# Kernel optimization log

Measured on AMD Instinct MI355X. Metric: run time of the kernel, lower is better.

The kernel has to match this reference:

```python
import jax, jax.numpy as jnp
import numpy as np

B, H, W, C, UNITS = 16, 64, 64, 64, 128

def setup_inputs() -> dict:
    key = jax.random.key(0)
    k1, k2 = jax.random.split(key)
    x = jax.random.normal(k1, (B, H, W, C), dtype=jnp.float32)
    # 'random_normal' keras initializer defaults to stddev=0.05
    w = jax.random.normal(k2, (UNITS, C, W, H), dtype=jnp.float32) * 0.05
    return {"x": x, "w": w}

def reference(x, w):
    # Original: transpose NHWC->NCHW, broadcasted matmul (W,H)@(H,W),
    # reduce-sum over C, transpose back, relu.
    # Fused contraction: y[b,i,j,u] = sum_{c,h} w[u,c,i,h] * x[b,h,j,c]
    y = jnp.einsum('ucih,bhjc->biju', w, x)  # (B, W, W, units)
    return jax.nn.relu(y)
```

## Files before the change

### kernel.cpp

```cpp
#include <hip/hip_runtime.h>
#include <hip/hip_bf16.h>


typedef __attribute__((ext_vector_type(4))) float f32x4;
typedef __attribute__((ext_vector_type(8))) short bf16x8;
typedef __attribute__((ext_vector_type(4))) unsigned int u32x4;
typedef __attribute__((ext_vector_type(2))) unsigned int u32x2;
typedef unsigned short ushort_t;

static __device__ __forceinline__ unsigned int cvt_pk_bf16(float lo, float hi) {
  unsigned int r;
  asm("v_cvt_pk_bf16_f32 %0, %1, %2" : "=v"(r) : "v"(lo), "v"(hi));
  return r;
}

static __device__ __forceinline__ void async_copy16(void* lds, const void* g) {
  __builtin_amdgcn_global_load_lds(
      (const __attribute__((address_space(1))) unsigned int*)g,
      (__attribute__((address_space(3))) unsigned int*)lds, 16, 0, 0);
}

__global__ __launch_bounds__(256)
void conv_x(const float* __restrict__ X, ushort_t* __restrict__ Xb, int n4) {
  int idx = blockIdx.x * 256 + threadIdx.x;
  const int stride = gridDim.x * 256;
  for (; idx < n4; idx += stride) {
    f32x4 v = ((const f32x4*)X)[idx];
    u32x2 o;
    o.x = cvt_pk_bf16(v.x, v.y);
    o.y = cvt_pk_bf16(v.z, v.w);
    ((u32x2*)Xb)[idx] = o;
  }
}

__global__ __launch_bounds__(256)
void conv_w(const float* __restrict__ W, ushort_t* __restrict__ Wb) {
  __shared__ float T[64][65];
  const int bid = blockIdx.x;
  const int u = bid >> 6;
  const int i = bid & 63;
  const int t = threadIdx.x;

  const int hq = t & 15;
  const int c4 = t >> 4;
  const float* base = W + (((size_t)u * 64) * 64 + i) * 64;
#pragma unroll
  for (int it = 0; it < 4; ++it) {
    const int c = it * 16 + c4;
    f32x4 v = *(const f32x4*)(base + (size_t)c * 4096 + hq * 4);
    *(f32x4*)&T[c][hq * 4] = v;
  }
  __syncthreads();

  const int h = t >> 2;
  const int c0 = (t & 3) * 16;
  unsigned int pk[8];
#pragma unroll
  for (int q = 0; q < 8; ++q)
    pk[q] = cvt_pk_bf16(T[c0 + 2 * q][h], T[c0 + 2 * q + 1][h]);
  ushort_t* out = Wb + (((size_t)i * 128 + u) * 64 + h) * 64 + c0;
  ((u32x4*)out)[0] = *(u32x4*)&pk[0];
  ((u32x4*)out)[1] = *(u32x4*)&pk[4];
}

__global__ __launch_bounds__(256, 2)
void gemm_bf16(const ushort_t* __restrict__ Xb, const ushort_t* __restrict__ Wb,
               float* __restrict__ O) {
  __shared__ ushort_t As[2][128 * 64];
  __shared__ ushort_t Bs[2][128 * 64];

  const int tid = threadIdx.x;
  const int lane = tid & 63;
  const int wid = tid >> 6;
  const int wm = wid >> 1;
  const int wn = wid & 1;

  const int bid = blockIdx.x;
  const int wg = (bid & 7) * 64 + (bid >> 3);
  const int mt = wg & 7;
  const int nt = wg >> 3;

  const char* XbB = (const char*)Xb;
  const char* WbB = (const char*)Wb;
  const int b0 = mt * 2;

  int a_bl[4], a_off[4], b_u[4], b_off[4];
#pragma unroll
  for (int it = 0; it < 4; ++it) {
    const int flat = it * 4096 + tid * 16;
    const int bl = flat >> 13;
    const int rem = flat & 8191;
    const int j = rem >> 7;
    const int slot = (rem >> 4) & 7;
    a_bl[it] = bl;
    a_off[it] = j * 128 + (slot ^ (j & 7)) * 16;
    const int u = flat >> 7;
    const int slotb = (flat >> 4) & 7;
    b_u[it] = u;
    b_off[it] = (slotb ^ (u & 7)) * 16;
  }

  f32x4 acc[4][4];
#pragma unroll
  for (int i = 0; i < 4; ++i)
#pragma unroll
    for (int j = 0; j < 4; ++j) acc[i][j] = (f32x4){0.f, 0.f, 0.f, 0.f};

  auto stage = [&](int buf, int h) {
    char* la = (char*)&As[buf][0];
    char* lb = (char*)&Bs[buf][0];
#pragma unroll
    for (int it = 0; it < 4; ++it) {
      const char* src =
          XbB + (size_t)((b0 + a_bl[it]) * 64 + h) * 8192 + a_off[it];
      async_copy16(la + it * 4096 + tid * 16, src);
    }
#pragma unroll
    for (int it = 0; it < 4; ++it) {
      const char* src =
          WbB + (size_t)((nt * 128 + b_u[it]) * 64 + h) * 128 + b_off[it];
      async_copy16(lb + it * 4096 + tid * 16, src);
    }
  };

  auto compute = [&](int buf) {
    const char* abase = (const char*)&As[buf][0];
    const char* bbase = (const char*)&Bs[buf][0];
#pragma unroll
    for (int kk = 0; kk < 2; ++kk) {
      bf16x8 af[4], bfr[4];
#pragma unroll
      for (int mf = 0; mf < 4; ++mf) {
        const int row = wm * 64 + mf * 16 + (lane & 15);
        const int byte0 = row * 128 + kk * 64 + (lane >> 4) * 16;
        af[mf] = *(const bf16x8*)(abase + (byte0 ^ ((row & 7) << 4)));
      }
#pragma unroll
      for (int nf = 0; nf < 4; ++nf) {
        const int row = wn * 64 + nf * 16 + (lane & 15);
        const int byte0 = row * 128 + kk * 64 + (lane >> 4) * 16;
        bfr[nf] = *(const bf16x8*)(bbase + (byte0 ^ ((row & 7) << 4)));
      }
#pragma unroll
      for (int mf = 0; mf < 4; ++mf)
#pragma unroll
        for (int nf = 0; nf < 4; ++nf)
          acc[mf][nf] = __builtin_amdgcn_mfma_f32_16x16x32_bf16(
              af[mf], bfr[nf], acc[mf][nf], 0, 0, 0);
    }
  };

  stage(0, 0);
  __syncthreads();
  int cur = 0;
  for (int t = 0; t < 64; ++t) {
    if (t < 63) stage(cur ^ 1, t + 1);
    compute(cur);
    __syncthreads();
    cur ^= 1;
  }

  const int rbase = (lane >> 4) * 4;
  const int cn = lane & 15;
#pragma unroll
  for (int mf = 0; mf < 4; ++mf) {
#pragma unroll
    for (int r = 0; r < 4; ++r) {
      const int ml = wm * 64 + mf * 16 + rbase + r;
      const int m = mt * 128 + ml;
      const int b = m >> 6;
      const int j = m & 63;
      float* orow = O + (((size_t)b * 64 + nt) * 64 + j) * 128;
#pragma unroll
      for (int nf = 0; nf < 4; ++nf) {
        const int u = wn * 64 + nf * 16 + cn;
        orow[u] = fmaxf(acc[mf][nf][r], 0.f);
      }
    }
  }
}

__global__ __launch_bounds__(256, 2)
void fused_gemm(const float* __restrict__ X, const float* __restrict__ Wt,
                float* __restrict__ O) {
  __shared__ ushort_t As[2][128 * 64];
  __shared__ ushort_t Bs[2][128 * 64];
  const int tid = threadIdx.x;
  const int lane = tid & 63;
  const int wid = tid >> 6;
  const int wm = wid >> 1;
  const int wn = wid & 1;
  const int bid = blockIdx.x;
  const int wg = (bid & 7) * 64 + (bid >> 3);
  const int mt = wg & 7;
  const int nt = wg >> 3;
  const int a_ml = tid >> 1;
  const int a_hp = (tid & 1) * 2;
  const int a_b = (mt * 128 + a_ml) >> 6;
  const int a_j = a_ml & 63;
  const float* a_base = X + ((size_t)a_b << 18) + ((size_t)a_j << 6);
  const int b_nl = tid >> 1;
  const int b_c8 = (tid & 1) * 8;
  const float* b_base = Wt + ((size_t)b_nl << 18) + ((size_t)nt << 6);
  f32x4 ra[2][4];
  f32x4 rb[8];
  f32x4 acc[4][4];
#pragma unroll
  for (int i = 0; i < 4; ++i)
#pragma unroll
    for (int j = 0; j < 4; ++j) acc[i][j] = (f32x4){0.f, 0.f, 0.f, 0.f};
  auto stage_load = [&](int t) {
    const int th = t & 15;
    const int tc = t >> 4;
    const int c0 = tc * 16;
    const int h0 = th * 4;
#pragma unroll
    for (int s = 0; s < 2; ++s) {
      const float* p = a_base + (size_t)(h0 + a_hp + s) * 4096 + c0;
#pragma unroll
      for (int q = 0; q < 4; ++q) ra[s][q] = ((const f32x4*)p)[q];
    }
#pragma unroll
    for (int q = 0; q < 8; ++q)
      rb[q] = *(const f32x4*)(b_base + (size_t)(c0 + b_c8 + q) * 4096 + h0);
  };
  auto stage_write = [&](int buf) {
    char* abase = (char*)&As[buf][0];
    const int swa = (a_ml & 7) << 4;
#pragma unroll
    for (int s = 0; s < 2; ++s) {
      u32x4 lo, hi;
      lo.x = cvt_pk_bf16(ra[s][0].x, ra[s][0].y);
      lo.y = cvt_pk_bf16(ra[s][0].z, ra[s][0].w);
      lo.z = cvt_pk_bf16(ra[s][1].x, ra[s][1].y);
      lo.w = cvt_pk_bf16(ra[s][1].z, ra[s][1].w);
      hi.x = cvt_pk_bf16(ra[s][2].x, ra[s][2].y);
      hi.y = cvt_pk_bf16(ra[s][2].z, ra[s][2].w);
      hi.z = cvt_pk_bf16(ra[s][3].x, ra[s][3].y);
      hi.w = cvt_pk_bf16(ra[s][3].z, ra[s][3].w);
      const int byte0 = a_ml * 128 + (a_hp + s) * 32;
      *(u32x4*)(abase + (byte0 ^ swa)) = lo;
      *(u32x4*)(abase + ((byte0 + 16) ^ swa)) = hi;
    }
    char* bbase = (char*)&Bs[buf][0];
    const int swb = (b_nl & 7) << 4;
#pragma unroll
    for (int hl = 0; hl < 4; ++hl) {
      u32x4 v;
      v.x = cvt_pk_bf16(rb[0][hl], rb[1][hl]);
      v.y = cvt_pk_bf16(rb[2][hl], rb[3][hl]);
      v.z = cvt_pk_bf16(rb[4][hl], rb[5][hl]);
      v.w = cvt_pk_bf16(rb[6][hl], rb[7][hl]);
      const int byte0 = b_nl * 128 + (hl * 16 + b_c8) * 2;
      *(u32x4*)(bbase + (byte0 ^ swb)) = v;
    }
  };
  auto compute = [&](int buf) {
    const char* abase = (const char*)&As[buf][0];
    const char* bbase = (const char*)&Bs[buf][0];
#pragma unroll
    for (int kk = 0; kk < 2; ++kk) {
      bf16x8 af[4], bfr[4];
#pragma unroll
      for (int mf = 0; mf < 4; ++mf) {
        const int row = wm * 64 + mf * 16 + (lane & 15);
        const int byte0 = row * 128 + kk * 64 + (lane >> 4) * 16;
        af[mf] = *(const bf16x8*)(abase + (byte0 ^ ((row & 7) << 4)));
      }
#pragma unroll
      for (int nf = 0; nf < 4; ++nf) {
        const int row = wn * 64 + nf * 16 + (lane & 15);
        const int byte0 = row * 128 + kk * 64 + (lane >> 4) * 16;
        bfr[nf] = *(const bf16x8*)(bbase + (byte0 ^ ((row & 7) << 4)));
      }
#pragma unroll
      for (int mf = 0; mf < 4; ++mf)
#pragma unroll
        for (int nf = 0; nf < 4; ++nf)
          acc[mf][nf] = __builtin_amdgcn_mfma_f32_16x16x32_bf16(
              af[mf], bfr[nf], acc[mf][nf], 0, 0, 0);
    }
  };
  stage_load(0);
  stage_write(0);
  __syncthreads();
  int cur = 0;
  for (int t = 0; t < 64; ++t) {
    if (t + 1 < 64) stage_load(t + 1);
    compute(cur);
    if (t + 1 < 64) stage_write(cur ^ 1);
    __syncthreads();
    cur ^= 1;
  }
  const int rbase = (lane >> 4) * 4;
  const int cn = lane & 15;
#pragma unroll
  for (int mf = 0; mf < 4; ++mf) {
#pragma unroll
    for (int r = 0; r < 4; ++r) {
      const int ml = wm * 64 + mf * 16 + rbase + r;
      const int m = mt * 128 + ml;
      const int b = m >> 6;
      const int j = m & 63;
      float* orow = O + (((size_t)b * 64 + nt) * 64 + j) * 128;
#pragma unroll
      for (int nf = 0; nf < 4; ++nf) {
        const int u = wn * 64 + nf * 16 + cn;
        orow[u] = fmaxf(acc[mf][nf][r], 0.f);
      }
    }
  }
}

extern "C" void kernel_launch(void* const* d_in, const int* in_sizes, int n_in,
                              void* d_out, int out_size, void* d_ws, size_t ws_size,
                              hipStream_t stream) {
  const float* x = (const float*)d_in[0];
  const float* w = (const float*)d_in[1];
  float* out = (float*)d_out;

  const size_t XB_BYTES = (size_t)16 * 64 * 64 * 64 * 2;
  const size_t WB_BYTES = (size_t)64 * 128 * 64 * 64 * 2;

  if (ws_size >= XB_BYTES + WB_BYTES) {
    ushort_t* Xb = (ushort_t*)d_ws;
    ushort_t* Wb = (ushort_t*)((char*)d_ws + XB_BYTES);
    hipLaunchKernelGGL(conv_x, dim3(2048), dim3(256), 0, stream, x, Xb,
                       (int)(16 * 64 * 64 * 64 / 4));
    hipLaunchKernelGGL(conv_w, dim3(8192), dim3(256), 0, stream, w, Wb);
    hipLaunchKernelGGL(gemm_bf16, dim3(512), dim3(256), 0, stream, Xb, Wb, out);
  } else {
    hipLaunchKernelGGL(fused_gemm, dim3(512), dim3(256), 0, stream, x, w, out);
  }
}
```

Measured before the change: 122.1 us.

## Use 8-wave 128x256 GEMM tile with triple-buffered split async prefetch

Replaces the 4-wave 128x128 double-buffered bf16 GEMM with an 8-wave kernel covering a 128x256 tile. It uses a three-deep LDS ring whose global-to-LDS prefetch is split across the two k-substeps, gated by explicit vmcnt waits and raw s_barriers. MFMA phases are raised with s_setprio, and LDS read offsets are precomputed. The aim is to hide load latency and cut per-step sync overhead, at the cost of more LDS (144KB) and only one block per CU. The conv_x launch grid is also halved.

```diff
diff --git a/kernel.cpp b/kernel.cpp
--- a/kernel.cpp
+++ b/kernel.cpp
@@ -63,41 +63,59 @@
   ((u32x4*)out)[1] = *(u32x4*)&pk[4];
 }
 
-__global__ __launch_bounds__(256, 2)
-void gemm_bf16(const ushort_t* __restrict__ Xb, const ushort_t* __restrict__ Wb,
-               float* __restrict__ O) {
-  __shared__ ushort_t As[2][128 * 64];
-  __shared__ ushort_t Bs[2][128 * 64];
+__global__ __launch_bounds__(512, 2)
+void gemm8(const ushort_t* __restrict__ Xb, const ushort_t* __restrict__ Wb,
+           float* __restrict__ O) {
+  __shared__ ushort_t As[3][128 * 64];
+  __shared__ ushort_t Bs[3][256 * 64];
 
   const int tid = threadIdx.x;
   const int lane = tid & 63;
   const int wid = tid >> 6;
-  const int wm = wid >> 1;
-  const int wn = wid & 1;
+  const int wm = wid >> 2;
+  const int wn = wid & 3;
 
   const int bid = blockIdx.x;
-  const int wg = (bid & 7) * 64 + (bid >> 3);
+  const int wg = (bid & 7) * 32 + (bid >> 3);
   const int mt = wg & 7;
-  const int nt = wg >> 3;
+  const int nt2 = wg >> 3;
 
   const char* XbB = (const char*)Xb;
   const char* WbB = (const char*)Wb;
-  const int b0 = mt * 2;
-
-  int a_bl[4], a_off[4], b_u[4], b_off[4];
+
+  int a_dst[2]; size_t a_src[2];
+#pragma unroll
+  for (int it = 0; it < 2; ++it) {
+    const int flat = it * 8192 + tid * 16;
+    const int row = flat >> 7;
+    const int p = (flat >> 4) & 7;
+    const int b = mt * 2 + (row >> 6);
+    const int j = row & 63;
+    a_dst[it] = flat;
+    a_src[it] = (size_t)b * 524288 + (size_t)j * 128 + ((p ^ (row & 7)) << 4);
+  }
+  int b_dst[4]; size_t b_src[4];
 #pragma unroll
   for (int it = 0; it < 4; ++it) {
-    const int flat = it * 4096 + tid * 16;
-    const int bl = flat >> 13;
-    const int rem = flat & 8191;
-    const int j = rem >> 7;
-    const int slot = (rem >> 4) & 7;
-    a_bl[it] = bl;
-    a_off[it] = j * 128 + (slot ^ (j & 7)) * 16;
-    const int u = flat >> 7;
-    const int slotb = (flat >> 4) & 7;
-    b_u[it] = u;
-    b_off[it] = (slotb ^ (u & 7)) * 16;
+    const int flat = it * 8192 + tid * 16;
+    const int nl = flat >> 7;
+    const int p = (flat >> 4) & 7;
+    b_dst[it] = flat;
+    b_src[it] = (size_t)(nt2 * 256 + nl) * 8192 + ((p ^ (nl & 7)) << 4);
+  }
+
+  int a_ro[2][4], b_ro[2][4];
+#pragma unroll
+  for (int kk = 0; kk < 2; ++kk) {
+#pragma unroll
+    for (int f = 0; f < 4; ++f) {
+      int row = wm * 64 + f * 16 + (lane & 15);
+      int byte0 = row * 128 + kk * 64 + (lane >> 4) * 16;
+      a_ro[kk][f] = byte0 ^ ((row & 7) << 4);
+      row = wn * 64 + f * 16 + (lane & 15);
+      byte0 = row * 128 + kk * 64 + (lane >> 4) * 16;
+      b_ro[kk][f] = byte0 ^ ((row & 7) << 4);
+    }
   }
 
   f32x4 acc[4][4];
@@ -106,58 +124,76 @@
 #pragma unroll
     for (int j = 0; j < 4; ++j) acc[i][j] = (f32x4){0.f, 0.f, 0.f, 0.f};
 
-  auto stage = [&](int buf, int h) {
+  auto stageA = [&](int buf, int h) {
     char* la = (char*)&As[buf][0];
+#pragma unroll
+    for (int it = 0; it < 2; ++it)
+      async_copy16(la + a_dst[it], XbB + a_src[it] + (size_t)h * 8192);
+  };
+  auto stageB0 = [&](int buf, int h) {
     char* lb = (char*)&Bs[buf][0];
-#pragma unroll
-    for (int it = 0; it < 4; ++it) {
-      const char* src =
-          XbB + (size_t)((b0 + a_bl[it]) * 64 + h) * 8192 + a_off[it];
-      async_copy16(la + it * 4096 + tid * 16, src);
-    }
-#pragma unroll
-    for (int it = 0; it < 4; ++it) {
-      const char* src =
-          WbB + (size_t)((nt * 128 + b_u[it]) * 64 + h) * 128 + b_off[it];
-      async_copy16(lb + it * 4096 + tid * 16, src);
-    }
-  };
-
-  auto compute = [&](int buf) {
-    const char* abase = (const char*)&As[buf][0];
-    const char* bbase = (const char*)&Bs[buf][0];
-#pragma unroll
-    for (int kk = 0; kk < 2; ++kk) {
-      bf16x8 af[4], bfr[4];
-#pragma unroll
-      for (int mf = 0; mf < 4; ++mf) {
-        const int row = wm * 64 + mf * 16 + (lane & 15);
-        const int byte0 = row * 128 + kk * 64 + (lane >> 4) * 16;
-        af[mf] = *(const bf16x8*)(abase + (byte0 ^ ((row & 7) << 4)));
-      }
-#pragma unroll
-      for (int nf = 0; nf < 4; ++nf) {
-        const int row = wn * 64 + nf * 16 + (lane & 15);
-        const int byte0 = row * 128 + kk * 64 + (lane >> 4) * 16;
-        bfr[nf] = *(const bf16x8*)(bbase + (byte0 ^ ((row & 7) << 4)));
-      }
-#pragma unroll
-      for (int mf = 0; mf < 4; ++mf)
-#pragma unroll
-        for (int nf = 0; nf < 4; ++nf)
-          acc[mf][nf] = __builtin_amdgcn_mfma_f32_16x16x32_bf16(
-              af[mf], bfr[nf], acc[mf][nf], 0, 0, 0);
-    }
-  };
-
-  stage(0, 0);
-  __syncthreads();
-  int cur = 0;
+    async_copy16(lb + b_dst[0], WbB + b_src[0] + (size_t)h * 128);
+  };
+  auto stageB123 = [&](int buf, int h) {
+    char* lb = (char*)&Bs[buf][0];
+#pragma unroll
+    for (int it = 1; it < 4; ++it)
+      async_copy16(lb + b_dst[it], WbB + b_src[it] + (size_t)h * 128);
+  };
+
+  stageA(0, 0); stageB0(0, 0); stageB123(0, 0);
+  stageA(1, 1); stageB0(1, 1); stageB123(1, 1);
+  asm volatile("s_waitcnt vmcnt(6)" ::: "memory");
+  __builtin_amdgcn_s_barrier();
+
+  int cur = 0, pre = 2;
   for (int t = 0; t < 64; ++t) {
-    if (t < 63) stage(cur ^ 1, t + 1);
-    compute(cur);
-    __syncthreads();
-    cur ^= 1;
+    const int h2 = t + 2;
+    const char* ab = (const char*)&As[cur][0];
+    const char* bb = (const char*)&Bs[cur][0];
+    bf16x8 af[4], bfr[4];
+
+    __builtin_amdgcn_sched_barrier(0);
+#pragma unroll
+    for (int f = 0; f < 4; ++f) af[f] = *(const bf16x8*)(ab + a_ro[0][f]);
+#pragma unroll
+    for (int f = 0; f < 4; ++f) bfr[f] = *(const bf16x8*)(bb + b_ro[0][f]);
+    if (h2 < 64) { stageA(pre, h2); stageB0(pre, h2); }
+    __builtin_amdgcn_s_barrier();
+    __builtin_amdgcn_s_setprio(1);
+#pragma unroll
+    for (int mf = 0; mf < 4; ++mf)
+#pragma unroll
+      for (int nf = 0; nf < 4; ++nf)
+        acc[mf][nf] = __builtin_amdgcn_mfma_f32_16x16x32_bf16(
+            af[mf], bfr[nf], acc[mf][nf], 0, 0, 0);
+    __builtin_amdgcn_s_setprio(0);
+    __builtin_amdgcn_s_barrier();
+
+    __builtin_amdgcn_sched_barrier(0);
+#pragma unroll
+    for (int f = 0; f < 4; ++f) af[f] = *(const bf16x8*)(ab + a_ro[1][f]);
+#pragma unroll
+    for (int f = 0; f < 4; ++f) bfr[f] = *(const bf16x8*)(bb + b_ro[1][f]);
+    if (h2 < 64) stageB123(pre, h2);
+    __builtin_amdgcn_s_barrier();
+    __builtin_amdgcn_s_setprio(1);
+#pragma unroll
+    for (int mf = 0; mf < 4; ++mf)
+#pragma unroll
+      for (int nf = 0; nf < 4; ++nf)
+        acc[mf][nf] = __builtin_amdgcn_mfma_f32_16x16x32_bf16(
+            af[mf], bfr[nf], acc[mf][nf], 0, 0, 0);
+    __builtin_amdgcn_s_setprio(0);
+    if (t < 62) {
+      asm volatile("s_waitcnt vmcnt(6)" ::: "memory");
+    } else {
+      asm volatile("s_waitcnt vmcnt(0)" ::: "memory");
+    }
+    __builtin_amdgcn_s_barrier();
+
+    cur = (cur == 2) ? 0 : cur + 1;
+    pre = (pre == 2) ? 0 : pre + 1;
   }
 
   const int rbase = (lane >> 4) * 4;
@@ -170,11 +206,12 @@
       const int m = mt * 128 + ml;
       const int b = m >> 6;
       const int j = m & 63;
-      float* orow = O + (((size_t)b * 64 + nt) * 64 + j) * 128;
 #pragma unroll
       for (int nf = 0; nf < 4; ++nf) {
-        const int u = wn * 64 + nf * 16 + cn;
-        orow[u] = fmaxf(acc[mf][nf][r], 0.f);
+        const int nloc = wn * 64 + nf * 16 + cn;
+        const int i = nt2 * 2 + (nloc >> 7);
+        const int u = nloc & 127;
+        O[(((size_t)b * 64 + i) * 64 + j) * 128 + u] = fmaxf(acc[mf][nf][r], 0.f);
       }
     }
   }
@@ -325,10 +362,10 @@
   if (ws_size >= XB_BYTES + WB_BYTES) {
     ushort_t* Xb = (ushort_t*)d_ws;
     ushort_t* Wb = (ushort_t*)((char*)d_ws + XB_BYTES);
-    hipLaunchKernelGGL(conv_x, dim3(2048), dim3(256), 0, stream, x, Xb,
+    hipLaunchKernelGGL(conv_x, dim3(1024), dim3(256), 0, stream, x, Xb,
                        (int)(16 * 64 * 64 * 64 / 4));
     hipLaunchKernelGGL(conv_w, dim3(8192), dim3(256), 0, stream, w, Wb);
-    hipLaunchKernelGGL(gemm_bf16, dim3(512), dim3(256), 0, stream, Xb, Wb, out);
+    hipLaunchKernelGGL(gemm8, dim3(256), dim3(512), 0, stream, Xb, Wb, out);
   } else {
     hipLaunchKernelGGL(fused_gemm, dim3(512), dim3(256), 0, stream, x, w, out);
   }
```

After: 109.6 us. 1.11x faster.
